# Kernel optimization log

Hardware: AMD Instinct MI355X
Metric: run time of the kernel (lower is better)

## Reference

```python
import jax, jax.numpy as jnp
import numpy as np

N, E = 50000, 800000
IN_DIM, E_DIM, OUT_DIM, H = 128, 32, 16, 4
NEG_SLOPE = 0.2


def setup_inputs() -> dict:
    key = jax.random.key(0)
    ks = jax.random.split(key, 9)
    return {
        "feat": jax.random.normal(ks[0], (N, IN_DIM), jnp.float32),
        "edge_attr": jax.random.normal(ks[1], (E, E_DIM), jnp.float32),
        "src": jax.random.randint(ks[2], (E,), 0, N),
        "dst": jax.random.randint(ks[3], (E,), 0, N),
        "W_fc": jax.random.normal(ks[4], (OUT_DIM * H, IN_DIM), jnp.float32) * 0.1,
        "W_edge": jax.random.normal(ks[5], (OUT_DIM * H, E_DIM), jnp.float32) * 0.1,
        "attn_h": jax.random.normal(ks[6], (1, H, OUT_DIM), jnp.float32) * 0.1,
        "attn_t": jax.random.normal(ks[7], (1, H, OUT_DIM), jnp.float32) * 0.1,
        "attn_e": jax.random.normal(ks[8], (1, H, OUT_DIM), jnp.float32) * 0.1,
        "bias": jnp.zeros((1, H, OUT_DIM), jnp.float32),
    }


def reference(feat, edge_attr, src, dst, W_fc, W_edge, attn_h, attn_t, attn_e, bias):
    n = feat.shape[0]
    # node / edge projections
    feat_ = (feat @ W_fc.T).reshape(n, H, OUT_DIM)          # [N,H,D]
    eh = (feat_ * attn_h).sum(-1)                            # [N,H]
    et = (feat_ * attn_t).sum(-1)                            # [N,H]
    feat_e = (edge_attr @ W_edge.T).reshape(-1, H, OUT_DIM)  # [E,H,D]
    ee = (feat_e * attn_e).sum(-1)                           # [E,H]
    # per-edge attention logits: u_add_e then e_add_v, then leaky relu
    e = eh[src] + ee + et[dst]                               # [E,H]
    e = jnp.where(e > 0, e, NEG_SLOPE * e)
    # edge softmax grouped by destination node
    e_max = jax.ops.segment_max(e, dst, num_segments=n)      # [N,H]
    e_max = jnp.where(jnp.isfinite(e_max), e_max, 0.0)
    a = jnp.exp(e - e_max[dst])                              # [E,H]
    a_sum = jax.ops.segment_sum(a, dst, num_segments=n)      # [N,H]
    a = a / jnp.where(a_sum[dst] > 0, a_sum[dst], 1.0)
    # u_mul_e + sum aggregation
    msg = feat_[src] * a[:, :, None]                         # [E,H,D]
    rst = jax.ops.segment_sum(msg, dst, num_segments=n)      # [N,H,D]
    rst = rst + bias
    return rst.reshape(n, H * OUT_DIM)                       # concat_out
```

## Files before the change

kernel.cpp:

```cpp
#include <hip/hip_runtime.h>

#define NN 50000
#define EE 800000
#define IND 128
#define EDD 32
#define ODD 16
#define NH 4
#define HD 64
#define NEG_SLOPE 0.2f
#define NBLK ((NN + 255) / 256)

__global__ __launch_bounds__(256)
void k_init(int* __restrict__ deg, int* __restrict__ cursor) {
    int i = blockIdx.x * 256 + threadIdx.x;
    if (i < NN) { deg[i] = 0; cursor[i] = 0; }
}

__global__ __launch_bounds__(256)
void k_prep(const float* __restrict__ W_fc, const float* __restrict__ W_edge,
            const float* __restrict__ attn_e,
            float* __restrict__ Wt, float* __restrict__ w_ee) {
    int i = blockIdx.x * 256 + threadIdx.x;
    if (i < HD * IND) {
        int k = i >> 6, j = i & 63;
        Wt[i] = W_fc[j * IND + k];
    }
    if (i < NH * EDD) {
        int h = i >> 5, k = i & 31;
        float s = 0.f;
        for (int d = 0; d < ODD; ++d)
            s += W_edge[(h * ODD + d) * EDD + k] * attn_e[h * ODD + d];
        w_ee[i] = s;
    }
}

__global__ __launch_bounds__(256)
void k_node(const float* __restrict__ feat, const float* __restrict__ Wt,
            const float* __restrict__ attn_h, const float* __restrict__ attn_t,
            float* __restrict__ feat_ws, float4* __restrict__ eh4,
            float4* __restrict__ et4) {
    int n = blockIdx.x * 256 + threadIdx.x;
    if (n >= NN) return;
    float acc[HD];
#pragma unroll
    for (int j = 0; j < HD; ++j) acc[j] = 0.f;
    const float* fr = feat + (long)n * IND;
#pragma unroll 1
    for (int k0 = 0; k0 < IND; k0 += 4) {
        float4 p = *(const float4*)(fr + k0);
        float f[4] = {p.x, p.y, p.z, p.w};
#pragma unroll
        for (int kk = 0; kk < 4; ++kk) {
            const float* w = Wt + (k0 + kk) * HD;
#pragma unroll
            for (int j = 0; j < HD; ++j) acc[j] += f[kk] * w[j];
        }
    }
    float4* d4 = (float4*)(feat_ws + (long)n * HD);
#pragma unroll
    for (int q = 0; q < 16; ++q)
        d4[q] = make_float4(acc[q*4], acc[q*4+1], acc[q*4+2], acc[q*4+3]);
    float sh[NH], st[NH];
#pragma unroll
    for (int h = 0; h < NH; ++h) {
        sh[h] = 0.f; st[h] = 0.f;
#pragma unroll
        for (int d = 0; d < ODD; ++d) {
            float av = acc[h * ODD + d];
            sh[h] += av * attn_h[h * ODD + d];
            st[h] += av * attn_t[h * ODD + d];
        }
    }
    eh4[n] = make_float4(sh[0], sh[1], sh[2], sh[3]);
    et4[n] = make_float4(st[0], st[1], st[2], st[3]);
}

__global__ __launch_bounds__(256)
void k_hist(const int* __restrict__ dst, int* __restrict__ deg) {
    int e = blockIdx.x * 256 + threadIdx.x;
    if (e < EE) atomicAdd(&deg[dst[e]], 1);
}

__global__ __launch_bounds__(256)
void k_scan1(const int* __restrict__ deg, int* __restrict__ offs, int* __restrict__ part) {
    __shared__ int s[256];
    int t = threadIdx.x, i = blockIdx.x * 256 + t;
    int v = (i < NN) ? deg[i] : 0;
    s[t] = v;
    __syncthreads();
#pragma unroll
    for (int o = 1; o < 256; o <<= 1) {
        int u = (t >= o) ? s[t - o] : 0;
        __syncthreads();
        if (t >= o) s[t] += u;
        __syncthreads();
    }
    if (i < NN) offs[i] = s[t] - v;
    if (t == 255) part[blockIdx.x] = s[255];
}

__global__ __launch_bounds__(256)
void k_scan2(int* __restrict__ part) {
    __shared__ int s[256];
    int t = threadIdx.x;
    int v = (t < NBLK) ? part[t] : 0;
    s[t] = v;
    __syncthreads();
#pragma unroll
    for (int o = 1; o < 256; o <<= 1) {
        int u = (t >= o) ? s[t - o] : 0;
        __syncthreads();
        if (t >= o) s[t] += u;
        __syncthreads();
    }
    if (t < NBLK) part[t] = s[t] - v;
}

__global__ __launch_bounds__(256)
void k_scan3(int* __restrict__ offs, const int* __restrict__ part) {
    int i = blockIdx.x * 256 + threadIdx.x;
    if (i < NN) offs[i] += part[i >> 8];
}

__global__ __launch_bounds__(256)
void k_logit(const float* __restrict__ edge_attr, const int* __restrict__ src,
             const int* __restrict__ dst, const float* __restrict__ w_ee,
             const float4* __restrict__ eh4, const float4* __restrict__ et4,
             const int* __restrict__ offs, int* __restrict__ cursor,
             float4* __restrict__ e_buf4, int* __restrict__ perm) {
    int e = blockIdx.x * 256 + threadIdx.x;
    if (e >= EE) return;
    int s_ = src[e], d_ = dst[e];
    int pos = offs[d_] + atomicAdd(&cursor[d_], 1);
    float4 vh = eh4[s_];
    float4 vt = et4[d_];
    const float* ea = edge_attr + (long)e * EDD;
    float f[EDD];
#pragma unroll
    for (int c = 0; c < 8; ++c) {
        float4 p = *(const float4*)(ea + c * 4);
        f[c*4+0] = p.x; f[c*4+1] = p.y; f[c*4+2] = p.z; f[c*4+3] = p.w;
    }
    float x[NH];
#pragma unroll
    for (int h = 0; h < NH; ++h) {
        float s = 0.f;
#pragma unroll
        for (int k = 0; k < EDD; ++k) s += f[k] * w_ee[h * EDD + k];
        x[h] = s;
    }
    x[0] += vh.x + vt.x; x[1] += vh.y + vt.y;
    x[2] += vh.z + vt.z; x[3] += vh.w + vt.w;
#pragma unroll
    for (int h = 0; h < NH; ++h) {
        float v = x[h];
        v = v > 0.f ? v : NEG_SLOPE * v;
        x[h] = __expf(v);
    }
    e_buf4[e] = make_float4(x[0], x[1], x[2], x[3]);
    perm[pos] = e;
}

__global__ __launch_bounds__(256)
void k_reduce(const int* __restrict__ offs, const int* __restrict__ deg,
              const float* __restrict__ e_buf, const int* __restrict__ perm,
              const int* __restrict__ src, const float* __restrict__ feat_ws,
              const float* __restrict__ bias, float* __restrict__ out) {
    int wid = (blockIdx.x * 256 + threadIdx.x) >> 6;
    int lane = threadIdx.x & 63;
    if (wid >= NN) return;
    int start = __builtin_amdgcn_readfirstlane(offs[wid]);
    int dn    = __builtin_amdgcn_readfirstlane(deg[wid]);
    int h = lane >> 4;
    float acc = 0.f, l = 0.f;
    int i = 0;
    for (; i + 2 <= dn; i += 2) {
        int e0 = perm[start + i];
        int e1 = perm[start + i + 1];
        int s0 = src[e0];
        int s1 = src[e1];
        float a0 = e_buf[(long)e0 * 4 + h];
        float a1 = e_buf[(long)e1 * 4 + h];
        float f0 = feat_ws[(long)s0 * HD + lane];
        float f1 = feat_ws[(long)s1 * HD + lane];
        l += a0 + a1;
        acc += a0 * f0;
        acc += a1 * f1;
    }
    if (i < dn) {
        int e0 = perm[start + i];
        int s0 = src[e0];
        float a0 = e_buf[(long)e0 * 4 + h];
        l += a0;
        acc += a0 * feat_ws[(long)s0 * HD + lane];
    }
    float res = (l > 0.f) ? acc / l : 0.f;
    out[(long)wid * HD + lane] = res + bias[lane];
}

extern "C" void kernel_launch(void* const* d_in, const int* in_sizes, int n_in,
                              void* d_out, int out_size, void* d_ws, size_t ws_size,
                              hipStream_t stream) {
    const float* feat      = (const float*)d_in[0];
    const float* edge_attr = (const float*)d_in[1];
    const int*   src       = (const int*)d_in[2];
    const int*   dst       = (const int*)d_in[3];
    const float* W_fc      = (const float*)d_in[4];
    const float* W_edge    = (const float*)d_in[5];
    const float* attn_h    = (const float*)d_in[6];
    const float* attn_t    = (const float*)d_in[7];
    const float* attn_e    = (const float*)d_in[8];
    const float* bias      = (const float*)d_in[9];
    float* out             = (float*)d_out;

    float* ws        = (float*)d_ws;
    float4* e_buf4   = (float4*)ws;
    float4* eh4      = e_buf4 + EE;
    float4* et4      = eh4 + NN;
    float*  feat_ws  = (float*)(et4 + NN);
    float*  Wt       = feat_ws + (long)NN * HD;
    float*  w_ee     = Wt + HD * IND;
    int*    perm     = (int*)(w_ee + NH * EDD);
    int*    deg      = perm + EE;
    int*    offs     = deg + NN;
    int*    cursor   = offs + NN;
    int*    part     = cursor + NN;

    k_init<<<NBLK, 256, 0, stream>>>(deg, cursor);
    k_prep<<<(HD * IND + 255) / 256, 256, 0, stream>>>(W_fc, W_edge, attn_e, Wt, w_ee);
    k_node<<<NBLK, 256, 0, stream>>>(feat, Wt, attn_h, attn_t, feat_ws, eh4, et4);
    k_hist<<<(EE + 255) / 256, 256, 0, stream>>>(dst, deg);
    k_scan1<<<NBLK, 256, 0, stream>>>(deg, offs, part);
    k_scan2<<<1, 256, 0, stream>>>(part);
    k_scan3<<<NBLK, 256, 0, stream>>>(offs, part);
    k_logit<<<(EE + 255) / 256, 256, 0, stream>>>(edge_attr, src, dst, w_ee, eh4, et4,
                                                  offs, cursor, e_buf4, perm);
    k_reduce<<<(NN * 64 + 255) / 256, 256, 0, stream>>>(offs, deg, (const float*)e_buf4,
                                                        perm, src, feat_ws, bias, out);
}
```

Measured before the change: 374.7 us.

## Reuse histogram ranks, split node GEMM per half, batch reduce gathers with shuffles

```diff
diff --git a/kernel.cpp b/kernel.cpp
--- a/kernel.cpp
+++ b/kernel.cpp
@@ -11,9 +11,9 @@
 #define NBLK ((NN + 255) / 256)
 
 __global__ __launch_bounds__(256)
-void k_init(int* __restrict__ deg, int* __restrict__ cursor) {
+void k_init(int* __restrict__ deg) {
     int i = blockIdx.x * 256 + threadIdx.x;
-    if (i < NN) { deg[i] = 0; cursor[i] = 0; }
+    if (i < NN) deg[i] = 0;
 }
 
 __global__ __launch_bounds__(256)
@@ -37,48 +37,51 @@
 __global__ __launch_bounds__(256)
 void k_node(const float* __restrict__ feat, const float* __restrict__ Wt,
             const float* __restrict__ attn_h, const float* __restrict__ attn_t,
-            float* __restrict__ feat_ws, float4* __restrict__ eh4,
-            float4* __restrict__ et4) {
-    int n = blockIdx.x * 256 + threadIdx.x;
+            float* __restrict__ feat_ws, float2* __restrict__ eh2,
+            float2* __restrict__ et2) {
+    int t = blockIdx.x * 256 + threadIdx.x;
+    int n = t >> 1, half = t & 1;
     if (n >= NN) return;
-    float acc[HD];
-#pragma unroll
-    for (int j = 0; j < HD; ++j) acc[j] = 0.f;
+    float acc[32];
+#pragma unroll
+    for (int j = 0; j < 32; ++j) acc[j] = 0.f;
     const float* fr = feat + (long)n * IND;
+    const int jbase = half * 32;
 #pragma unroll 1
     for (int k0 = 0; k0 < IND; k0 += 4) {
         float4 p = *(const float4*)(fr + k0);
         float f[4] = {p.x, p.y, p.z, p.w};
 #pragma unroll
         for (int kk = 0; kk < 4; ++kk) {
-            const float* w = Wt + (k0 + kk) * HD;
-#pragma unroll
-            for (int j = 0; j < HD; ++j) acc[j] += f[kk] * w[j];
-        }
-    }
-    float4* d4 = (float4*)(feat_ws + (long)n * HD);
-#pragma unroll
-    for (int q = 0; q < 16; ++q)
+            const float* w = Wt + (k0 + kk) * HD + jbase;
+#pragma unroll
+            for (int j = 0; j < 32; ++j) acc[j] += f[kk] * w[j];
+        }
+    }
+    float4* d4 = (float4*)(feat_ws + (long)n * HD + jbase);
+#pragma unroll
+    for (int q = 0; q < 8; ++q)
         d4[q] = make_float4(acc[q*4], acc[q*4+1], acc[q*4+2], acc[q*4+3]);
-    float sh[NH], st[NH];
-#pragma unroll
-    for (int h = 0; h < NH; ++h) {
-        sh[h] = 0.f; st[h] = 0.f;
+    float sh[2], st[2];
+#pragma unroll
+    for (int hh = 0; hh < 2; ++hh) {
+        sh[hh] = 0.f; st[hh] = 0.f;
+        int hg = half * 2 + hh;
 #pragma unroll
         for (int d = 0; d < ODD; ++d) {
-            float av = acc[h * ODD + d];
-            sh[h] += av * attn_h[h * ODD + d];
-            st[h] += av * attn_t[h * ODD + d];
-        }
-    }
-    eh4[n] = make_float4(sh[0], sh[1], sh[2], sh[3]);
-    et4[n] = make_float4(st[0], st[1], st[2], st[3]);
-}
-
-__global__ __launch_bounds__(256)
-void k_hist(const int* __restrict__ dst, int* __restrict__ deg) {
+            float av = acc[hh * ODD + d];
+            sh[hh] += av * attn_h[hg * ODD + d];
+            st[hh] += av * attn_t[hg * ODD + d];
+        }
+    }
+    eh2[n * 2 + half] = make_float2(sh[0], sh[1]);
+    et2[n * 2 + half] = make_float2(st[0], st[1]);
+}
+
+__global__ __launch_bounds__(256)
+void k_hist(const int* __restrict__ dst, int* __restrict__ deg, int* __restrict__ rank) {
     int e = blockIdx.x * 256 + threadIdx.x;
-    if (e < EE) atomicAdd(&deg[dst[e]], 1);
+    if (e < EE) rank[e] = atomicAdd(&deg[dst[e]], 1);
 }
 
 __global__ __launch_bounds__(256)
@@ -126,12 +129,12 @@
 void k_logit(const float* __restrict__ edge_attr, const int* __restrict__ src,
              const int* __restrict__ dst, const float* __restrict__ w_ee,
              const float4* __restrict__ eh4, const float4* __restrict__ et4,
-             const int* __restrict__ offs, int* __restrict__ cursor,
+             const int* __restrict__ offs, const int* __restrict__ rank,
              float4* __restrict__ e_buf4, int* __restrict__ perm) {
     int e = blockIdx.x * 256 + threadIdx.x;
     if (e >= EE) return;
     int s_ = src[e], d_ = dst[e];
-    int pos = offs[d_] + atomicAdd(&cursor[d_], 1);
+    int pos = offs[d_] + rank[e];
     float4 vh = eh4[s_];
     float4 vt = et4[d_];
     const float* ea = edge_attr + (long)e * EDD;
@@ -172,27 +175,27 @@
     int start = __builtin_amdgcn_readfirstlane(offs[wid]);
     int dn    = __builtin_amdgcn_readfirstlane(deg[wid]);
     int h = lane >> 4;
+    int q = lane & 15;
     float acc = 0.f, l = 0.f;
-    int i = 0;
-    for (; i + 2 <= dn; i += 2) {
-        int e0 = perm[start + i];
-        int e1 = perm[start + i + 1];
-        int s0 = src[e0];
-        int s1 = src[e1];
-        float a0 = e_buf[(long)e0 * 4 + h];
-        float a1 = e_buf[(long)e1 * 4 + h];
-        float f0 = feat_ws[(long)s0 * HD + lane];
-        float f1 = feat_ws[(long)s1 * HD + lane];
-        l += a0 + a1;
-        acc += a0 * f0;
-        acc += a1 * f1;
-    }
-    if (i < dn) {
-        int e0 = perm[start + i];
-        int s0 = src[e0];
-        float a0 = e_buf[(long)e0 * 4 + h];
-        l += a0;
-        acc += a0 * feat_ws[(long)s0 * HD + lane];
+
+    for (int c0 = 0; c0 < dn; c0 += 16) {
+        int rem = dn - c0; if (rem > 16) rem = 16;
+        int qq = (q < rem) ? q : (rem - 1);
+        int   e_q = perm[start + c0 + qq];
+        int   s_q = src[e_q];
+        float a_q = (q < rem) ? e_buf[(long)e_q * 4 + h] : 0.f;
+        float f[16];
+#pragma unroll
+        for (int i = 0; i < 16; ++i) {
+            int si = __shfl(s_q, i);
+            f[i] = feat_ws[(long)si * HD + lane];
+        }
+#pragma unroll
+        for (int i = 0; i < 16; ++i) {
+            float ai = __shfl(a_q, (lane & 48) + i);
+            l += ai;
+            acc += ai * f[i];
+        }
     }
     float res = (l > 0.f) ? acc / l : 0.f;
     out[(long)wid * HD + lane] = res + bias[lane];
@@ -221,20 +224,21 @@
     float*  Wt       = feat_ws + (long)NN * HD;
     float*  w_ee     = Wt + HD * IND;
     int*    perm     = (int*)(w_ee + NH * EDD);
-    int*    deg      = perm + EE;
+    int*    rank     = perm + EE;
+    int*    deg      = rank + EE;
     int*    offs     = deg + NN;
-    int*    cursor   = offs + NN;
-    int*    part     = cursor + NN;
-
-    k_init<<<NBLK, 256, 0, stream>>>(deg, cursor);
+    int*    part     = offs + NN;
+
+    k_init<<<NBLK, 256, 0, stream>>>(deg);
     k_prep<<<(HD * IND + 255) / 256, 256, 0, stream>>>(W_fc, W_edge, attn_e, Wt, w_ee);
-    k_node<<<NBLK, 256, 0, stream>>>(feat, Wt, attn_h, attn_t, feat_ws, eh4, et4);
-    k_hist<<<(EE + 255) / 256, 256, 0, stream>>>(dst, deg);
+    k_node<<<(NN * 2 + 255) / 256, 256, 0, stream>>>(feat, Wt, attn_h, attn_t, feat_ws,
+                                                     (float2*)eh4, (float2*)et4);
+    k_hist<<<(EE + 255) / 256, 256, 0, stream>>>(dst, deg, rank);
     k_scan1<<<NBLK, 256, 0, stream>>>(deg, offs, part);
     k_scan2<<<1, 256, 0, stream>>>(part);
     k_scan3<<<NBLK, 256, 0, stream>>>(offs, part);
     k_logit<<<(EE + 255) / 256, 256, 0, stream>>>(edge_attr, src, dst, w_ee, eh4, et4,
-                                                  offs, cursor, e_buf4, perm);
+                                                  offs, rank, e_buf4, perm);
     k_reduce<<<(NN * 64 + 255) / 256, 256, 0, stream>>>(offs, deg, (const float*)e_buf4,
                                                         perm, src, feat_ws, bias, out);
 }
```

Measured after the change: 426.0 us. 1.14x slower.
